# Kernel optimization log

Measured on AMD Instinct MI355X. Metric: run time of the kernel, lower is better.

Reference implementation:

```python
import jax, jax.numpy as jnp
from jax import lax
import numpy as np

B, C, L = 32, 8, 512
C_IN = 512      # must equal L (tokenConv consumes permuted tensor)
D_MODEL = 512
SCALE_NUM = 64  # 63 actual scales


def build_wavelet_bank(scale_num, LB=-8.0, UB=8.0, N=1024, Fb=2.0, Fc=8.0):
    """Replicates cmor_torch; returns centered zero-padded kernel bank [S, K].
    Zero-centering is exact because every kernel length (16*s+1) is odd and K is odd,
    so the padded conv with pad=(K-1)//2 equals the original per-scale conv with
    pad=(k-1)//2."""
    x = np.linspace(LB, UB, N)
    wav = (np.pi * Fb) ** (-0.5) * np.exp(2j * np.pi * Fc * x) * np.exp(-x ** 2 / Fb)
    step = x[1] - x[0]
    kernels = []
    for scale in np.arange(1, scale_num):
        j = (np.arange(scale * (x[-1] - x[0]) + 1) / (scale * step)).astype(int)
        j = j[j < wav.size]
        kernels.append(np.real(wav[j]) * scale ** (-0.5))
    K = max(len(k) for k in kernels)
    if K % 2 == 0:
        K += 1
    bank = np.zeros((len(kernels), K), np.float32)
    for i, k in enumerate(kernels):
        assert (K - len(k)) % 2 == 0, "kernel parity mismatch"
        off = (K - len(k)) // 2
        bank[i, off:off + len(k)] = k
    return bank


def setup_inputs() -> dict:
    key = jax.random.key(0)
    k1, k2 = jax.random.split(key)
    x = jax.random.normal(k1, (B, C, L), dtype=jnp.float32)
    wavelet_bank = jnp.asarray(build_wavelet_bank(SCALE_NUM))  # [63, K]
    token_w = jax.random.normal(k2, (D_MODEL, C_IN, 3), dtype=jnp.float32) * 0.02
    return {"x": x, "wavelet_bank": wavelet_bank, "token_w": token_w}


def reference(x, wavelet_bank, token_w):
    Bb, Cc, Ll = x.shape
    S, K = wavelet_bank.shape
    pad = (K - 1) // 2
    # fused CWT over all (channel, scale) pairs: [B*C, 1, L] conv [S, 1, K] -> [B*C, S, L]
    xr = x.reshape(Bb * Cc, 1, Ll)
    conv = lax.conv_general_dilated(
        xr, wavelet_bank[:, None, :], window_strides=(1,),
        padding=[(pad, pad)], dimension_numbers=("NCH", "OIH", "NCH"))
    d = jnp.abs(jnp.diff(conv, axis=-1))                 # [B*C, S, L-1]
    d = jnp.concatenate([d, d[..., -1:]], axis=-1)       # replicate last sample -> L
    feats = d.reshape(Bb, Cc * S, Ll)
    out = jnp.concatenate([x, feats], axis=1)            # [B, C*(1+S), L]
    # tokenConv on permuted tensor: channels = L (= c_in), length = C*(1+S)
    h = out.transpose(0, 2, 1)                           # [B, L, C_total]
    hp = jnp.concatenate([h[..., -1:], h, h[..., :1]], axis=-1)  # circular pad=1
    y = lax.conv_general_dilated(
        hp, token_w, window_strides=(1,), padding="VALID",
        dimension_numbers=("NCH", "OIH", "NCH"))         # [B, d_model, C_total]
    return y.transpose(0, 2, 1)                          # [B, C_total, d_model]
```

## Files before the change

### kernel.cpp

```cpp
#include <hip/hip_runtime.h>
#include <hip/hip_bf16.h>

#define NB 32
#define NC 8
#define NL 512
#define NS 63
#define NK 1009
#define NPAD 504
#define ND 512
#define NCT 512
#define NROWS 514

typedef __attribute__((ext_vector_type(4))) float f32x4;
typedef __attribute__((ext_vector_type(8))) short short8;
typedef __attribute__((ext_vector_type(4))) short short4v;

#define APAD_BYTES (NB * NROWS * NL * 2)
#define WB_BYTES   (3 * ND * NL * 2)
#define BANKB_BYTES (64 * 1024 * 2)

typedef const __attribute__((address_space(1))) unsigned int* gp1_t;
typedef __attribute__((address_space(3))) unsigned int* lp3_t;
__device__ __forceinline__ void gload_lds16(const void* g, void* l) {
  __builtin_amdgcn_global_load_lds((gp1_t)g, (lp3_t)l, 16, 0, 0);
}

__device__ __forceinline__ unsigned short bf16_bits(float v) {
  return __builtin_bit_cast(unsigned short, __float2bfloat16(v));
}

#define WAITVM(N) asm volatile("s_waitcnt vmcnt(" #N ")" ::: "memory")
#define FENCE() asm volatile("" ::: "memory")
#define BAR() __builtin_amdgcn_s_barrier()

__global__ __launch_bounds__(256) void prep_kernel(
    const float* __restrict__ bank, const float* __restrict__ tw,
    __hip_bfloat16* __restrict__ Wb, __hip_bfloat16* __restrict__ bankB) {
  const int idx = blockIdx.x * 256 + threadIdx.x;

  {
    int i0 = idx * 4;
    const float4* t4 = (const float4*)(tw + (size_t)i0 * 3);
    float4 a = t4[0], bq = t4[1], c4 = t4[2];
    ushort4 w0 = make_ushort4(bf16_bits(a.x), bf16_bits(a.w), bf16_bits(bq.z), bf16_bits(c4.y));
    ushort4 w1 = make_ushort4(bf16_bits(a.y), bf16_bits(bq.x), bf16_bits(bq.w), bf16_bits(c4.z));
    ushort4 w2 = make_ushort4(bf16_bits(a.z), bf16_bits(bq.y), bf16_bits(c4.x), bf16_bits(c4.w));
    *(ushort4*)(Wb + 0 * ND * NL + i0) = w0;
    *(ushort4*)(Wb + 1 * ND * NL + i0) = w1;
    *(ushort4*)(Wb + 2 * ND * NL + i0) = w2;
  }
  {
    int s = idx >> 10, k = idx & 1023;
    float v = (s < NS && k < NK) ? bank[s * NK + k] : 0.f;
    bankB[idx] = __float2bfloat16(v);
  }
}

#define CPY_STRIDE 3088

__global__ __launch_bounds__(512) void cwt_kernel(
    const float* __restrict__ x, const __hip_bfloat16* __restrict__ bankB,
    __hip_bfloat16* __restrict__ Apad) {
  __shared__ char smem[8 * 16384 + 4 * CPY_STRIDE];
  char* bankS = smem;
  char* cpy = smem + 8 * 16384;

  const int tid = threadIdx.x;
  const int bc = blockIdx.x;
  const int b = bc >> 3, c = bc & 7;
  const int w = tid >> 6, l = tid & 63;
  const int hi = l >> 4, li = l & 15;

  const float* xrow = x + bc * NL;

  if (tid < 512) {
    __hip_bfloat16 v = __float2bfloat16(xrow[tid]);
    Apad[((size_t)(b * NROWS) + 1 + c) * NL + tid] = v;
    if (c == 0) Apad[((size_t)(b * NROWS) + 513) * NL + tid] = v;
  }

  for (int i = 0; i < 6; ++i) {
    int p = tid + i * 512;
    int r_ = p / 768, pe = p - r_ * 768;
    int e0 = 2 * pe;
    int i0 = e0 + r_;
    float xa = (i0 >= NPAD && i0 < NPAD + NL) ? xrow[i0 - NPAD] : 0.f;
    float xb = (i0 + 1 >= NPAD && i0 + 1 < NPAD + NL) ? xrow[i0 + 1 - NPAD] : 0.f;
    float xc = (i0 + 2 >= NPAD && i0 + 2 < NPAD + NL) ? xrow[i0 + 2 - NPAD] : 0.f;
    unsigned short u0 = bf16_bits(xb - xa);
    unsigned short u1 = bf16_bits(xc - xb);
    *(unsigned int*)(cpy + r_ * CPY_STRIDE + e0 * 2) = (unsigned)u0 | ((unsigned)u1 << 16);
  }

#define STAGE(kt)                                                             \
  {                                                                           \
    for (int i = 0; i < 2; ++i) {                                             \
      int ck = tid + i * 512;                                                 \
      int s_ = ck >> 4, rb = ck & 15;                                         \
      int srcc = rb ^ (s_ & 7);                                               \
      gload_lds16(bankB + s_ * 1024 + (kt) * 128 + srcc * 8,                  \
                  bankS + (kt) * 16384 + ck * 16);                            \
    }                                                                         \
  }

#define CCOMP(kt)                                                              \
  {                                                                            \
    _Pragma("unroll") for (int ksl = 0; ksl < 4; ++ksl) {                      \
      short8 av[4], bv[4];                                                     \
      _Pragma("unroll") for (int m = 0; m < 4; ++m) {                          \
        int srow = m * 16 + li;                                                \
        int chunk = (ksl * 4 + hi) ^ (srow & 7);                               \
        av[m] = *(const short8*)(bankS + (kt) * 16384 + srow * 256 + chunk * 16); \
      }                                                                        \
      _Pragma("unroll") for (int n = 0; n < 4; ++n) {                          \
        int t = tbase + n * 16 + li;                                           \
        int e = t - r + (kt) * 128 + ksl * 32 + hi * 8;                        \
        const char* pc = cpy + r * CPY_STRIDE + e * 2;                         \
        short4v lo = *(const short4v*)pc;                                      \
        short4v hh = *(const short4v*)(pc + 8);                                \
        short8 f;                                                              \
        f[0] = lo[0]; f[1] = lo[1]; f[2] = lo[2]; f[3] = lo[3];                \
        f[4] = hh[0]; f[5] = hh[1]; f[6] = hh[2]; f[7] = hh[3];                \
        bv[n] = f;                                                             \
      }                                                                        \
      _Pragma("unroll") for (int m = 0; m < 4; ++m)                            \
        _Pragma("unroll") for (int n = 0; n < 4; ++n)                          \
          acc[m][n] = __builtin_amdgcn_mfma_f32_16x16x32_bf16(av[m], bv[n],    \
                                                              acc[m][n], 0, 0, 0); \
    }                                                                          \
  }

  STAGE(0); STAGE(1); STAGE(2); STAGE(3);
  STAGE(4); STAGE(5); STAGE(6); STAGE(7);

  f32x4 acc[4][4] = {};
  const int r = l & 3;
  const int tbase = w * 64;

  asm volatile("s_waitcnt vmcnt(14) lgkmcnt(0)" ::: "memory");
  BAR(); FENCE(); CCOMP(0);
  WAITVM(12); BAR(); FENCE(); CCOMP(1);
  WAITVM(10); BAR(); FENCE(); CCOMP(2);
  WAITVM(8);  BAR(); FENCE(); CCOMP(3);
  WAITVM(6);  BAR(); FENCE(); CCOMP(4);
  WAITVM(4);  BAR(); FENCE(); CCOMP(5);
  WAITVM(2);  BAR(); FENCE(); CCOMP(6);
  WAITVM(0);  BAR(); FENCE(); CCOMP(7);

#pragma unroll
  for (int m = 0; m < 4; ++m) {
#pragma unroll
    for (int rg = 0; rg < 4; ++rg) {
      int s = m * 16 + hi * 4 + rg;
      if (s >= NS) continue;
      int ch = 8 + c * NS + s;
      size_t rowbase = ((size_t)(b * NROWS) + 1 + ch) * NL;
#pragma unroll
      for (int n = 0; n < 4; ++n) {
        int t = tbase + n * 16 + li;
        float d = fabsf(acc[m][n][rg]);
        __hip_bfloat16 hv = __float2bfloat16(d);
        bool lastgrp = (w == 7 && n == 3);
        bool skip = lastgrp && (li == 15);
        bool dup = lastgrp && (li == 14);
        if (!skip) Apad[rowbase + t] = hv;
        if (dup) Apad[rowbase + 511] = hv;
        if (ch == NCT - 1) {
          size_t wrapbase = (size_t)(b * NROWS) * NL;
          if (!skip) Apad[wrapbase + t] = hv;
          if (dup) Apad[wrapbase + 511] = hv;
        }
      }
    }
  }
#undef STAGE
#undef CCOMP
}

__global__ __launch_bounds__(256) void gemm_kernel(
    const __hip_bfloat16* __restrict__ Ap, const __hip_bfloat16* __restrict__ Wb,
    float* __restrict__ out) {
  __shared__ __hip_bfloat16 sA[4][128 * 32];
  __shared__ __hip_bfloat16 sB[4][128 * 32];

  const int tid = threadIdx.x;
  const int gid = blockIdx.x;
  const int q = gid >> 3;
  const int pid = (gid & 7) * 16 + (q >> 2);
  const int b = pid >> 2;
  const int p0 = (pid & 3) * 128;
  const int o0 = (q & 3) * 128;

  const int w = tid >> 6, lane = tid & 63;
  const int wm = w >> 1, wn = w & 1;
  const int row_in = lane & 15, hi = lane >> 4;

  const int r0 = tid >> 2, cg0 = (tid & 3) ^ ((r0 >> 1) & 3);
  const int ck1 = tid + 256;
  const int r1 = ck1 >> 2, cg1 = (ck1 & 3) ^ ((r1 >> 1) & 3);

#define GSTAGE(kk, bu)                                                         \
  {                                                                            \
    const int kap_ = (kk) >> 4;                                                \
    const int l0_ = ((kk) & 15) << 5;                                          \
    gload_lds16(Ap + ((b * NROWS + p0 + kap_ + r0) * NL + l0_ + cg0 * 8),      \
                &sA[bu][tid * 8]);                                             \
    gload_lds16(Ap + ((b * NROWS + p0 + kap_ + r1) * NL + l0_ + cg1 * 8),      \
                &sA[bu][ck1 * 8]);                                             \
    gload_lds16(Wb + ((kap_ * ND + o0 + r0) * NL + l0_ + cg0 * 8),             \
                &sB[bu][tid * 8]);                                             \
    gload_lds16(Wb + ((kap_ * ND + o0 + r1) * NL + l0_ + cg1 * 8),             \
                &sB[bu][ck1 * 8]);                                             \
  }

#define COMPUTE(bu)                                                            \
  {                                                                            \
    short8 av[4], bv[4];                                                       \
    _Pragma("unroll") for (int m = 0; m < 4; ++m) {                            \
      int row = wm * 64 + m * 16 + row_in;                                     \
      int slot = row * 4 + (hi ^ ((row >> 1) & 3));                            \
      av[m] = *(const short8*)(&sA[bu][slot * 8]);                             \
    }                                                                          \
    _Pragma("unroll") for (int n = 0; n < 4; ++n) {                            \
      int row = wn * 64 + n * 16 + row_in;                                     \
      int slot = row * 4 + (hi ^ ((row >> 1) & 3));                            \
      bv[n] = *(const short8*)(&sB[bu][slot * 8]);                             \
    }                                                                          \
    _Pragma("unroll") for (int m = 0; m < 4; ++m)                              \
      _Pragma("unroll") for (int n = 0; n < 4; ++n)                            \
        acc[m][n] = __builtin_amdgcn_mfma_f32_16x16x32_bf16(av[m], bv[n],      \
                                                            acc[m][n], 0, 0, 0); \
  }

  f32x4 acc[4][4] = {};

  GSTAGE(0, 0);
  GSTAGE(1, 1);

  for (int g = 0; g < 11; ++g) {
    const int kk = g * 4;
    GSTAGE(kk + 2, 2); WAITVM(8); BAR(); FENCE(); COMPUTE(0);
    GSTAGE(kk + 3, 3); WAITVM(8); BAR(); FENCE(); COMPUTE(1);
    GSTAGE(kk + 4, 0); WAITVM(8); BAR(); FENCE(); COMPUTE(2);
    GSTAGE(kk + 5, 1); WAITVM(8); BAR(); FENCE(); COMPUTE(3);
  }
  GSTAGE(46, 2); WAITVM(8); BAR(); FENCE(); COMPUTE(0);
  GSTAGE(47, 3); WAITVM(8); BAR(); FENCE(); COMPUTE(1);
  WAITVM(4); BAR(); FENCE(); COMPUTE(2);
  WAITVM(0); BAR(); FENCE(); COMPUTE(3);
#undef GSTAGE
#undef COMPUTE

#pragma unroll
  for (int m = 0; m < 4; ++m) {
    const int p = p0 + wm * 64 + m * 16 + hi * 4;
#pragma unroll
    for (int n = 0; n < 4; ++n) {
      const int o = o0 + wn * 64 + n * 16 + row_in;
#pragma unroll
      for (int r = 0; r < 4; ++r)
        out[(size_t)((b * NCT) + p + r) * ND + o] = acc[m][n][r];
    }
  }
}

extern "C" void kernel_launch(void* const* d_in, const int* in_sizes, int n_in,
                              void* d_out, int out_size, void* d_ws, size_t ws_size,
                              hipStream_t stream) {
  const float* x = (const float*)d_in[0];
  const float* bank = (const float*)d_in[1];
  const float* tw = (const float*)d_in[2];
  float* out = (float*)d_out;

  char* ws = (char*)d_ws;
  __hip_bfloat16* Apad = (__hip_bfloat16*)ws;
  __hip_bfloat16* Wb = (__hip_bfloat16*)(ws + APAD_BYTES);
  __hip_bfloat16* bankB = (__hip_bfloat16*)(ws + APAD_BYTES + WB_BYTES);

  prep_kernel<<<256, 256, 0, stream>>>(bank, tw, Wb, bankB);
  cwt_kernel<<<256, 512, 0, stream>>>(x, bankB, Apad);
  gemm_kernel<<<512, 256, 0, stream>>>(Apad, Wb, out);
}
```

Baseline: 62.74 us.

## Split CWT scales across two blocks and reuse A tile across GEMM taps

The CWT kernel now launches twice as many blocks, each handling two of the four 16-scale groups, balanced so the sparse outer k-tiles (zero-padded bank regions) are skipped per group. This halves the LDS footprint and raises occupancy. The GEMM kernel now loads one A tile per k-step and reuses it for all three conv taps via shifted row reads, with two boundary rows staged separately, rather than reloading A for each tap. The cost is a larger B staging buffer, more complex indexing and a two-stage pipeline with an extra barrier per iteration.

New measurement: 62.42 us. No clear change (-0.5%).

```diff
diff --git a/kernel.cpp b/kernel.cpp
--- a/kernel.cpp
+++ b/kernel.cpp
@@ -61,22 +61,26 @@
 __global__ __launch_bounds__(512) void cwt_kernel(
     const float* __restrict__ x, const __hip_bfloat16* __restrict__ bankB,
     __hip_bfloat16* __restrict__ Apad) {
-  __shared__ char smem[8 * 16384 + 4 * CPY_STRIDE];
+  __shared__ char smem[8 * 8192 + 4 * CPY_STRIDE];
   char* bankS = smem;
-  char* cpy = smem + 8 * 16384;
+  char* cpy = smem + 8 * 8192;
 
   const int tid = threadIdx.x;
-  const int bc = blockIdx.x;
+  const int gid = blockIdx.x;
+  const int bc = gid >> 1, h = gid & 1;
   const int b = bc >> 3, c = bc & 7;
   const int w = tid >> 6, l = tid & 63;
   const int hi = l >> 4, li = l & 15;
+  const int ma = h ? 1 : 0, mb = h ? 2 : 3;
 
   const float* xrow = x + bc * NL;
 
-  if (tid < 512) {
-    __hip_bfloat16 v = __float2bfloat16(xrow[tid]);
-    Apad[((size_t)(b * NROWS) + 1 + c) * NL + tid] = v;
-    if (c == 0) Apad[((size_t)(b * NROWS) + 513) * NL + tid] = v;
+  if (h == 0) {
+    __hip_bfloat16 v = __float2bfloat16(xrow[tid & 511]);
+    if (tid < 512) {
+      Apad[((size_t)(b * NROWS) + 1 + c) * NL + tid] = v;
+      if (c == 0) Apad[((size_t)(b * NROWS) + 513) * NL + tid] = v;
+    }
   }
 
   for (int i = 0; i < 6; ++i) {
@@ -94,24 +98,17 @@
 
 #define STAGE(kt)                                                             \
   {                                                                           \
-    for (int i = 0; i < 2; ++i) {                                             \
-      int ck = tid + i * 512;                                                 \
-      int s_ = ck >> 4, rb = ck & 15;                                         \
-      int srcc = rb ^ (s_ & 7);                                               \
-      gload_lds16(bankB + s_ * 1024 + (kt) * 128 + srcc * 8,                  \
-                  bankS + (kt) * 16384 + ck * 16);                            \
-    }                                                                         \
-  }
-
-#define CCOMP(kt)                                                              \
+    int s_ = tid >> 4, rb = tid & 15;                                         \
+    int j = (s_ < 16) ? (ma * 16 + s_) : (mb * 16 + (s_ - 16));               \
+    int srcc = rb ^ (s_ & 7);                                                 \
+    gload_lds16(bankB + j * 1024 + (kt) * 128 + srcc * 8,                     \
+                bankS + (kt) * 8192 + tid * 16);                              \
+  }
+
+#define CCOMP(kt, A0, A1)                                                      \
   {                                                                            \
     _Pragma("unroll") for (int ksl = 0; ksl < 4; ++ksl) {                      \
-      short8 av[4], bv[4];                                                     \
-      _Pragma("unroll") for (int m = 0; m < 4; ++m) {                          \
-        int srow = m * 16 + li;                                                \
-        int chunk = (ksl * 4 + hi) ^ (srow & 7);                               \
-        av[m] = *(const short8*)(bankS + (kt) * 16384 + srow * 256 + chunk * 16); \
-      }                                                                        \
+      short8 bv[4];                                                            \
       _Pragma("unroll") for (int n = 0; n < 4; ++n) {                          \
         int t = tbase + n * 16 + li;                                           \
         int e = t - r + (kt) * 128 + ksl * 32 + hi * 8;                        \
@@ -123,42 +120,67 @@
         f[4] = hh[0]; f[5] = hh[1]; f[6] = hh[2]; f[7] = hh[3];                \
         bv[n] = f;                                                             \
       }                                                                        \
-      _Pragma("unroll") for (int m = 0; m < 4; ++m)                            \
+      if (A0) {                                                                \
+        int lrow = li;                                                         \
+        int chunk = (ksl * 4 + hi) ^ (lrow & 7);                               \
+        short8 av = *(const short8*)(bankS + (kt) * 8192 + lrow * 256 + chunk * 16); \
         _Pragma("unroll") for (int n = 0; n < 4; ++n)                          \
-          acc[m][n] = __builtin_amdgcn_mfma_f32_16x16x32_bf16(av[m], bv[n],    \
-                                                              acc[m][n], 0, 0, 0); \
+          acc[0][n] = __builtin_amdgcn_mfma_f32_16x16x32_bf16(av, bv[n],       \
+                                                              acc[0][n], 0, 0, 0); \
+      }                                                                        \
+      if (A1) {                                                                \
+        int lrow = 16 + li;                                                    \
+        int chunk = (ksl * 4 + hi) ^ (lrow & 7);                               \
+        short8 av = *(const short8*)(bankS + (kt) * 8192 + lrow * 256 + chunk * 16); \
+        _Pragma("unroll") for (int n = 0; n < 4; ++n)                          \
+          acc[1][n] = __builtin_amdgcn_mfma_f32_16x16x32_bf16(av, bv[n],       \
+                                                              acc[1][n], 0, 0, 0); \
+      }                                                                        \
     }                                                                          \
   }
 
-  STAGE(0); STAGE(1); STAGE(2); STAGE(3);
-  STAGE(4); STAGE(5); STAGE(6); STAGE(7);
-
-  f32x4 acc[4][4] = {};
+  f32x4 acc[2][4] = {};
   const int r = l & 3;
   const int tbase = w * 64;
 
-  asm volatile("s_waitcnt vmcnt(14) lgkmcnt(0)" ::: "memory");
-  BAR(); FENCE(); CCOMP(0);
-  WAITVM(12); BAR(); FENCE(); CCOMP(1);
-  WAITVM(10); BAR(); FENCE(); CCOMP(2);
-  WAITVM(8);  BAR(); FENCE(); CCOMP(3);
-  WAITVM(6);  BAR(); FENCE(); CCOMP(4);
-  WAITVM(4);  BAR(); FENCE(); CCOMP(5);
-  WAITVM(2);  BAR(); FENCE(); CCOMP(6);
-  WAITVM(0);  BAR(); FENCE(); CCOMP(7);
-
-#pragma unroll
-  for (int m = 0; m < 4; ++m) {
+  if (h == 0) {
+    STAGE(0); STAGE(1); STAGE(2); STAGE(3);
+    STAGE(4); STAGE(5); STAGE(6); STAGE(7);
+    asm volatile("s_waitcnt vmcnt(7) lgkmcnt(0)" ::: "memory");
+    BAR(); FENCE(); CCOMP(0, 0, 1);
+    WAITVM(6); BAR(); FENCE(); CCOMP(1, 0, 1);
+    WAITVM(5); BAR(); FENCE(); CCOMP(2, 1, 1);
+    WAITVM(4); BAR(); FENCE(); CCOMP(3, 1, 1);
+    WAITVM(3); BAR(); FENCE(); CCOMP(4, 1, 1);
+    WAITVM(2); BAR(); FENCE(); CCOMP(5, 0, 1);
+    WAITVM(1); BAR(); FENCE(); CCOMP(6, 0, 1);
+    WAITVM(0); BAR(); FENCE(); CCOMP(7, 0, 1);
+  } else {
+    STAGE(0); STAGE(1); STAGE(2); STAGE(3);
+    STAGE(4); STAGE(5); STAGE(6);
+    asm volatile("s_waitcnt vmcnt(6) lgkmcnt(0)" ::: "memory");
+    BAR(); FENCE(); CCOMP(0, 0, 1);
+    WAITVM(5); BAR(); FENCE(); CCOMP(1, 1, 1);
+    WAITVM(4); BAR(); FENCE(); CCOMP(2, 1, 1);
+    WAITVM(3); BAR(); FENCE(); CCOMP(3, 1, 1);
+    WAITVM(2); BAR(); FENCE(); CCOMP(4, 1, 1);
+    WAITVM(1); BAR(); FENCE(); CCOMP(5, 1, 1);
+    WAITVM(0); BAR(); FENCE(); CCOMP(6, 0, 1);
+  }
+
+#pragma unroll
+  for (int mm = 0; mm < 2; ++mm) {
+    const int mblk = mm ? mb : ma;
 #pragma unroll
     for (int rg = 0; rg < 4; ++rg) {
-      int s = m * 16 + hi * 4 + rg;
-      if (s >= NS) continue;
-      int ch = 8 + c * NS + s;
+      int jg = mblk * 16 + hi * 4 + rg;
+      if (jg >= NS) continue;
+      int ch = 8 + c * NS + jg;
       size_t rowbase = ((size_t)(b * NROWS) + 1 + ch) * NL;
 #pragma unroll
       for (int n = 0; n < 4; ++n) {
         int t = tbase + n * 16 + li;
-        float d = fabsf(acc[m][n][rg]);
+        float d = fabsf(acc[mm][n][rg]);
         __hip_bfloat16 hv = __float2bfloat16(d);
         bool lastgrp = (w == 7 && n == 3);
         bool skip = lastgrp && (li == 15);
@@ -180,8 +202,10 @@
 __global__ __launch_bounds__(256) void gemm_kernel(
     const __hip_bfloat16* __restrict__ Ap, const __hip_bfloat16* __restrict__ Wb,
     float* __restrict__ out) {
-  __shared__ __hip_bfloat16 sA[4][128 * 32];
-  __shared__ __hip_bfloat16 sB[4][128 * 32];
+  __shared__ char sAr[2 * 8192];
+  __shared__ char sBr[2 * 24576];
+  __shared__ char bnd[2048];
+  __shared__ char dump[2048];
 
   const int tid = threadIdx.x;
   const int gid = blockIdx.x;
@@ -195,59 +219,77 @@
   const int wm = w >> 1, wn = w & 1;
   const int row_in = lane & 15, hi = lane >> 4;
 
-  const int r0 = tid >> 2, cg0 = (tid & 3) ^ ((r0 >> 1) & 3);
+  const int rA0 = tid >> 2, cgA0 = (tid & 3) ^ ((rA0 >> 1) & 3);
   const int ck1 = tid + 256;
-  const int r1 = ck1 >> 2, cg1 = (ck1 & 3) ^ ((r1 >> 1) & 3);
+  const int rA1 = ck1 >> 2, cgA1 = (ck1 & 3) ^ ((rA1 >> 1) & 3);
+
+  {
+    int r_ = (tid >> 6) & 1;
+    int col = tid & 63;
+    const __hip_bfloat16* src =
+        Ap + ((size_t)(b * NROWS) + p0 + 128 + r_) * NL + col * 8;
+    char* dst = (tid < 128) ? (bnd + tid * 16) : (dump + (tid - 128) * 16);
+    gload_lds16(src, dst);
+  }
 
 #define GSTAGE(kk, bu)                                                         \
   {                                                                            \
-    const int kap_ = (kk) >> 4;                                                \
-    const int l0_ = ((kk) & 15) << 5;                                          \
-    gload_lds16(Ap + ((b * NROWS + p0 + kap_ + r0) * NL + l0_ + cg0 * 8),      \
-                &sA[bu][tid * 8]);                                             \
-    gload_lds16(Ap + ((b * NROWS + p0 + kap_ + r1) * NL + l0_ + cg1 * 8),      \
-                &sA[bu][ck1 * 8]);                                             \
-    gload_lds16(Wb + ((kap_ * ND + o0 + r0) * NL + l0_ + cg0 * 8),             \
-                &sB[bu][tid * 8]);                                             \
-    gload_lds16(Wb + ((kap_ * ND + o0 + r1) * NL + l0_ + cg1 * 8),             \
-                &sB[bu][ck1 * 8]);                                             \
-  }
-
-#define COMPUTE(bu)                                                            \
+    const int l0_ = (kk) * 32;                                                 \
+    gload_lds16(Ap + ((b * NROWS + p0 + rA0) * NL + l0_ + cgA0 * 8),           \
+                sAr + (bu) * 8192 + tid * 16);                                 \
+    gload_lds16(Ap + ((b * NROWS + p0 + rA1) * NL + l0_ + cgA1 * 8),           \
+                sAr + (bu) * 8192 + ck1 * 16);                                 \
+    _Pragma("unroll") for (int g = 0; g < 6; ++g) {                            \
+      int id = g * 256 + tid;                                                  \
+      int kap_ = id >> 9, ckb = id & 511;                                      \
+      int row = ckb >> 2, cg = (ckb & 3) ^ ((row >> 1) & 3);                   \
+      gload_lds16(Wb + ((kap_ * ND + o0 + row) * NL + l0_ + cg * 8),           \
+                  sBr + (bu) * 24576 + id * 16);                               \
+    }                                                                          \
+  }
+
+#define COMPUTE(bu, kk)                                                        \
   {                                                                            \
-    short8 av[4], bv[4];                                                       \
-    _Pragma("unroll") for (int m = 0; m < 4; ++m) {                            \
-      int row = wm * 64 + m * 16 + row_in;                                     \
-      int slot = row * 4 + (hi ^ ((row >> 1) & 3));                            \
-      av[m] = *(const short8*)(&sA[bu][slot * 8]);                             \
+    const int l0_ = (kk) * 32;                                                 \
+    _Pragma("unroll") for (int kap_ = 0; kap_ < 3; ++kap_) {                   \
+      short8 av[4], bv[4];                                                     \
+      _Pragma("unroll") for (int m = 0; m < 4; ++m) {                          \
+        int arow = wm * 64 + m * 16 + row_in + kap_;                           \
+        const char* pa;                                                        \
+        if (m == 3) {                                                          \
+          pa = (arow < 128)                                                    \
+             ? (sAr + (bu) * 8192 + (arow * 4 + (hi ^ ((arow >> 1) & 3))) * 16)\
+             : (bnd + (arow - 128) * 1024 + (l0_ + hi * 8) * 2);               \
+        } else {                                                               \
+          pa = sAr + (bu) * 8192 + (arow * 4 + (hi ^ ((arow >> 1) & 3))) * 16; \
+        }                                                                      \
+        av[m] = *(const short8*)pa;                                            \
+      }                                                                        \
+      _Pragma("unroll") for (int n = 0; n < 4; ++n) {                          \
+        int brow = wn * 64 + n * 16 + row_in;                                  \
+        bv[n] = *(const short8*)(sBr + (bu) * 24576 + kap_ * 8192 +            \
+                                 (brow * 4 + (hi ^ ((brow >> 1) & 3))) * 16);  \
+      }                                                                        \
+      _Pragma("unroll") for (int m = 0; m < 4; ++m)                            \
+        _Pragma("unroll") for (int n = 0; n < 4; ++n)                          \
+          acc[m][n] = __builtin_amdgcn_mfma_f32_16x16x32_bf16(av[m], bv[n],    \
+                                                              acc[m][n], 0, 0, 0); \
     }                                                                          \
-    _Pragma("unroll") for (int n = 0; n < 4; ++n) {                            \
-      int row = wn * 64 + n * 16 + row_in;                                     \
-      int slot = row * 4 + (hi ^ ((row >> 1) & 3));                            \
-      bv[n] = *(const short8*)(&sB[bu][slot * 8]);                             \
-    }                                                                          \
-    _Pragma("unroll") for (int m = 0; m < 4; ++m)                              \
-      _Pragma("unroll") for (int n = 0; n < 4; ++n)                            \
-        acc[m][n] = __builtin_amdgcn_mfma_f32_16x16x32_bf16(av[m], bv[n],      \
-                                                            acc[m][n], 0, 0, 0); \
   }
 
   f32x4 acc[4][4] = {};
 
   GSTAGE(0, 0);
-  GSTAGE(1, 1);
-
-  for (int g = 0; g < 11; ++g) {
-    const int kk = g * 4;
-    GSTAGE(kk + 2, 2); WAITVM(8); BAR(); FENCE(); COMPUTE(0);
-    GSTAGE(kk + 3, 3); WAITVM(8); BAR(); FENCE(); COMPUTE(1);
-    GSTAGE(kk + 4, 0); WAITVM(8); BAR(); FENCE(); COMPUTE(2);
-    GSTAGE(kk + 5, 1); WAITVM(8); BAR(); FENCE(); COMPUTE(3);
-  }
-  GSTAGE(46, 2); WAITVM(8); BAR(); FENCE(); COMPUTE(0);
-  GSTAGE(47, 3); WAITVM(8); BAR(); FENCE(); COMPUTE(1);
-  WAITVM(4); BAR(); FENCE(); COMPUTE(2);
-  WAITVM(0); BAR(); FENCE(); COMPUTE(3);
+
+  for (int kk = 0; kk < 15; ++kk) {
+    GSTAGE(kk + 1, (kk + 1) & 1);
+    WAITVM(8);
+    BAR(); FENCE();
+    COMPUTE(kk & 1, kk);
+    FENCE(); BAR();
+  }
+  WAITVM(0); BAR(); FENCE();
+  COMPUTE(1, 15);
 #undef GSTAGE
 #undef COMPUTE
 
@@ -278,6 +320,6 @@
   __hip_bfloat16* bankB = (__hip_bfloat16*)(ws + APAD_BYTES + WB_BYTES);
 
   prep_kernel<<<256, 256, 0, stream>>>(bank, tw, Wb, bankB);
-  cwt_kernel<<<256, 512, 0, stream>>>(x, bankB, Apad);
+  cwt_kernel<<<512, 512, 0, stream>>>(x, bankB, Apad);
   gemm_kernel<<<512, 256, 0, stream>>>(Apad, Wb, out);
 }
```

## Skip zero-band MFMAs in CWT, add setprio, deepen GEMM pipeline to five stages

Applied to the files above, without the earlier changes.

In the CWT kernel, the per-k-tile compute now skips MFMA row-blocks whose banded wavelet coefficients are zero for that k-tile, which trims matrix work on the sparse edges of the kernel bank. MFMA bursts in both kernels are wrapped in s_setprio to favour the math-issuing wave. The GEMM moves from a 4-buffer to a 5-buffer LDS ring with three tiles in flight, so load latency overlaps compute further. The cost is more LDS per block, which may lower occupancy, and the skip pattern relies on the specific bank layout.

Measured after the change: 66.25 us. +5.6%, slower.

```diff
diff --git a/kernel.cpp b/kernel.cpp
--- a/kernel.cpp
+++ b/kernel.cpp
@@ -32,6 +32,8 @@
 #define WAITVM(N) asm volatile("s_waitcnt vmcnt(" #N ")" ::: "memory")
 #define FENCE() asm volatile("" ::: "memory")
 #define BAR() __builtin_amdgcn_s_barrier()
+#define PRIO1() __builtin_amdgcn_s_setprio(1)
+#define PRIO0() __builtin_amdgcn_s_setprio(0)
 
 __global__ __launch_bounds__(256) void prep_kernel(
     const float* __restrict__ bank, const float* __restrict__ tw,
@@ -103,15 +105,20 @@
     }                                                                         \
   }
 
-#define CCOMP(kt)                                                              \
+#define AVMM(kt, ksl, m)                                                       \
+  {                                                                            \
+    int srow = (m) * 16 + li;                                                  \
+    int chunk = ((ksl) * 4 + hi) ^ (srow & 7);                                 \
+    short8 av = *(const short8*)(bankS + (kt) * 16384 + srow * 256 + chunk * 16); \
+    _Pragma("unroll") for (int n = 0; n < 4; ++n)                              \
+      acc[m][n] = __builtin_amdgcn_mfma_f32_16x16x32_bf16(av, bv[n],           \
+                                                          acc[m][n], 0, 0, 0); \
+  }
+
+#define CCOMP(kt, M0, M1, M2, M3)                                              \
   {                                                                            \
     _Pragma("unroll") for (int ksl = 0; ksl < 4; ++ksl) {                      \
-      short8 av[4], bv[4];                                                     \
-      _Pragma("unroll") for (int m = 0; m < 4; ++m) {                          \
-        int srow = m * 16 + li;                                                \
-        int chunk = (ksl * 4 + hi) ^ (srow & 7);                               \
-        av[m] = *(const short8*)(bankS + (kt) * 16384 + srow * 256 + chunk * 16); \
-      }                                                                        \
+      short8 bv[4];                                                            \
       _Pragma("unroll") for (int n = 0; n < 4; ++n) {                          \
         int t = tbase + n * 16 + li;                                           \
         int e = t - r + (kt) * 128 + ksl * 32 + hi * 8;                        \
@@ -123,10 +130,12 @@
         f[4] = hh[0]; f[5] = hh[1]; f[6] = hh[2]; f[7] = hh[3];                \
         bv[n] = f;                                                             \
       }                                                                        \
-      _Pragma("unroll") for (int m = 0; m < 4; ++m)                            \
-        _Pragma("unroll") for (int n = 0; n < 4; ++n)                          \
-          acc[m][n] = __builtin_amdgcn_mfma_f32_16x16x32_bf16(av[m], bv[n],    \
-                                                              acc[m][n], 0, 0, 0); \
+      PRIO1();                                                                 \
+      if (M0) AVMM(kt, ksl, 0);                                                \
+      if (M1) AVMM(kt, ksl, 1);                                                \
+      if (M2) AVMM(kt, ksl, 2);                                                \
+      if (M3) AVMM(kt, ksl, 3);                                                \
+      PRIO0();                                                                 \
     }                                                                          \
   }
 
@@ -138,14 +147,14 @@
   const int tbase = w * 64;
 
   asm volatile("s_waitcnt vmcnt(14) lgkmcnt(0)" ::: "memory");
-  BAR(); FENCE(); CCOMP(0);
-  WAITVM(12); BAR(); FENCE(); CCOMP(1);
-  WAITVM(10); BAR(); FENCE(); CCOMP(2);
-  WAITVM(8);  BAR(); FENCE(); CCOMP(3);
-  WAITVM(6);  BAR(); FENCE(); CCOMP(4);
-  WAITVM(4);  BAR(); FENCE(); CCOMP(5);
-  WAITVM(2);  BAR(); FENCE(); CCOMP(6);
-  WAITVM(0);  BAR(); FENCE(); CCOMP(7);
+  BAR(); FENCE(); CCOMP(0, 0, 0, 1, 1);
+  WAITVM(12); BAR(); FENCE(); CCOMP(1, 0, 1, 1, 1);
+  WAITVM(10); BAR(); FENCE(); CCOMP(2, 1, 1, 1, 1);
+  WAITVM(8);  BAR(); FENCE(); CCOMP(3, 1, 1, 1, 1);
+  WAITVM(6);  BAR(); FENCE(); CCOMP(4, 1, 1, 1, 1);
+  WAITVM(4);  BAR(); FENCE(); CCOMP(5, 0, 1, 1, 1);
+  WAITVM(2);  BAR(); FENCE(); CCOMP(6, 0, 0, 1, 1);
+  WAITVM(0);  BAR(); FENCE(); CCOMP(7, 0, 0, 0, 1);
 
 #pragma unroll
   for (int m = 0; m < 4; ++m) {
@@ -174,14 +183,15 @@
     }
   }
 #undef STAGE
+#undef AVMM
 #undef CCOMP
 }
 
 __global__ __launch_bounds__(256) void gemm_kernel(
     const __hip_bfloat16* __restrict__ Ap, const __hip_bfloat16* __restrict__ Wb,
     float* __restrict__ out) {
-  __shared__ __hip_bfloat16 sA[4][128 * 32];
-  __shared__ __hip_bfloat16 sB[4][128 * 32];
+  __shared__ __hip_bfloat16 sA[5][128 * 32];
+  __shared__ __hip_bfloat16 sB[5][128 * 32];
 
   const int tid = threadIdx.x;
   const int gid = blockIdx.x;
@@ -226,30 +236,35 @@
       int slot = row * 4 + (hi ^ ((row >> 1) & 3));                            \
       bv[n] = *(const short8*)(&sB[bu][slot * 8]);                             \
     }                                                                          \
+    PRIO1();                                                                   \
     _Pragma("unroll") for (int m = 0; m < 4; ++m)                              \
       _Pragma("unroll") for (int n = 0; n < 4; ++n)                            \
         acc[m][n] = __builtin_amdgcn_mfma_f32_16x16x32_bf16(av[m], bv[n],      \
                                                             acc[m][n], 0, 0, 0); \
-  }
+    PRIO0();                                                                   \
+  }
+
+#define STEP(kk, bu, bs)                                                       \
+  GSTAGE((kk) + 3, bs); WAITVM(12); BAR(); FENCE(); COMPUTE(bu); FENCE();
 
   f32x4 acc[4][4] = {};
 
-  GSTAGE(0, 0);
-  GSTAGE(1, 1);
-
-  for (int g = 0; g < 11; ++g) {
-    const int kk = g * 4;
-    GSTAGE(kk + 2, 2); WAITVM(8); BAR(); FENCE(); COMPUTE(0);
-    GSTAGE(kk + 3, 3); WAITVM(8); BAR(); FENCE(); COMPUTE(1);
-    GSTAGE(kk + 4, 0); WAITVM(8); BAR(); FENCE(); COMPUTE(2);
-    GSTAGE(kk + 5, 1); WAITVM(8); BAR(); FENCE(); COMPUTE(3);
-  }
-  GSTAGE(46, 2); WAITVM(8); BAR(); FENCE(); COMPUTE(0);
-  GSTAGE(47, 3); WAITVM(8); BAR(); FENCE(); COMPUTE(1);
-  WAITVM(4); BAR(); FENCE(); COMPUTE(2);
-  WAITVM(0); BAR(); FENCE(); COMPUTE(3);
+  GSTAGE(0, 0); GSTAGE(1, 1); GSTAGE(2, 2);
+
+  for (int g = 0; g < 9; ++g) {
+    const int kk = g * 5;
+    STEP(kk + 0, 0, 3);
+    STEP(kk + 1, 1, 4);
+    STEP(kk + 2, 2, 0);
+    STEP(kk + 3, 3, 1);
+    STEP(kk + 4, 4, 2);
+  }
+  WAITVM(8); BAR(); FENCE(); COMPUTE(0); FENCE();
+  WAITVM(4); BAR(); FENCE(); COMPUTE(1); FENCE();
+  WAITVM(0); BAR(); FENCE(); COMPUTE(2);
 #undef GSTAGE
 #undef COMPUTE
+#undef STEP
 
 #pragma unroll
   for (int m = 0; m < 4; ++m) {
```
